# Performance work log

Measured on AMD Instinct MI355X. Metric: run time of the kernel, lower is better.

The kernel has to match this reference:

```python
import jax, jax.numpy as jnp
import numpy as np
import math

N_EMBD = 768
N_HEAD = 12
B, T = 4, 2048
HEAD_DIM = N_EMBD // N_HEAD


def new_gelu(x):
    # GPT-2 tanh approximation of GELU (NewGELUActivation)
    c = math.sqrt(2.0 / math.pi)
    return 0.5 * x * (1.0 + jnp.tanh(c * (x + 0.044715 * jnp.power(x, 3.0))))


def layer_norm(x, g, b, eps=1e-5):
    mu = jnp.mean(x, axis=-1, keepdims=True)
    var = jnp.mean(jnp.square(x - mu), axis=-1, keepdims=True)
    return (x - mu) * jax.lax.rsqrt(var + eps) * g + b


def setup_inputs() -> dict:
    key = jax.random.key(0)
    ks = jax.random.split(key, 12)
    s = 0.02
    return {
        "x": jax.random.normal(ks[0], (B, T, N_EMBD), dtype=jnp.float32),
        "ln1_g": jnp.ones((N_EMBD,), jnp.float32),
        "ln1_b": jnp.zeros((N_EMBD,), jnp.float32),
        "W_attn": jax.random.normal(ks[1], (N_EMBD, 3 * N_EMBD), jnp.float32) * s,
        "b_attn": jnp.zeros((3 * N_EMBD,), jnp.float32),
        "W_proj": jax.random.normal(ks[2], (N_EMBD, N_EMBD), jnp.float32) * s,
        "b_proj": jnp.zeros((N_EMBD,), jnp.float32),
        "ln2_g": jnp.ones((N_EMBD,), jnp.float32),
        "ln2_b": jnp.zeros((N_EMBD,), jnp.float32),
        "W_fc": jax.random.normal(ks[3], (N_EMBD, 4 * N_EMBD), jnp.float32) * s,
        "b_fc": jnp.zeros((4 * N_EMBD,), jnp.float32),
        "W_fc2": jax.random.normal(ks[4], (4 * N_EMBD, N_EMBD), jnp.float32) * s,
        "b_fc2": jnp.zeros((N_EMBD,), jnp.float32),
    }


def block_forward(x, ln1_g, ln1_b, W_attn, b_attn, W_proj, b_proj,
                  ln2_g, ln2_b, W_fc, b_fc, W_fc2, b_fc2):
    # ---- attention sublayer (pre-LN) ----
    h = layer_norm(x, ln1_g, ln1_b)
    qkv = h @ W_attn + b_attn                      # [B,T,3C]
    q, k, v = jnp.split(qkv, 3, axis=-1)
    q = q.reshape(B, T, N_HEAD, HEAD_DIM).transpose(0, 2, 1, 3)  # [B,H,T,D]
    k = k.reshape(B, T, N_HEAD, HEAD_DIM).transpose(0, 2, 1, 3)
    v = v.reshape(B, T, N_HEAD, HEAD_DIM).transpose(0, 2, 1, 3)
    scores = jnp.einsum('bhqd,bhkd->bhqk', q, k) / math.sqrt(HEAD_DIM)
    causal = jnp.tril(jnp.ones((T, T), dtype=bool))
    scores = jnp.where(causal[None, None, :, :], scores, -jnp.inf)
    attn = jax.nn.softmax(scores, axis=-1)
    y = jnp.einsum('bhqk,bhkd->bhqd', attn, v)      # [B,H,T,D]
    y = y.transpose(0, 2, 1, 3).reshape(B, T, N_EMBD)
    y = y @ W_proj + b_proj
    x = x + y
    # ---- MLP sublayer ----
    h = layer_norm(x, ln2_g, ln2_b)
    h = new_gelu(h @ W_fc + b_fc)
    h = h @ W_fc2 + b_fc2
    return x + h


def reference(x, ln1_g, ln1_b, W_attn, b_attn, W_proj, b_proj,
              ln2_g, ln2_b, W_fc, b_fc, W_fc2, b_fc2):
    return block_forward(x, ln1_g, ln1_b, W_attn, b_attn, W_proj, b_proj,
                         ln2_g, ln2_b, W_fc, b_fc, W_fc2, b_fc2)
```

## Files before the change

### kernel.cpp

```cpp
#include <hip/hip_runtime.h>
#include <hip/hip_bf16.h>

typedef __attribute__((ext_vector_type(8))) short short8;
typedef __attribute__((ext_vector_type(4))) float f32x4;
typedef __attribute__((ext_vector_type(8))) unsigned short u16x8;
typedef __attribute__((ext_vector_type(4))) unsigned short u16x4;

#define MFMA16(A, B, C) __builtin_amdgcn_mfma_f32_16x16x32_bf16(A, B, C, 0, 0, 0)

static __device__ __forceinline__ unsigned short f2bf(float f) {
    unsigned int u = __builtin_bit_cast(unsigned int, f);
    u += 0x7FFF + ((u >> 16) & 1);
    return (unsigned short)(u >> 16);
}

static __device__ __forceinline__ unsigned int cvt_pk_bf16(float a, float b) {
    unsigned int r;
    asm("v_cvt_pk_bf16_f32 %0, %1, %2" : "=v"(r) : "v"(a), "v"(b));
    return r;
}

static __device__ __forceinline__ float gelu_f(float v) {
    const float k1 = 2.3022077646f;
    const float k2 = 0.1029432207f;
    float t = __builtin_amdgcn_exp2f(-(k1 * v + k2 * v * v * v));
    return v * __builtin_amdgcn_rcpf(1.0f + t);
}

typedef const __attribute__((address_space(1))) unsigned int* gas_t;
typedef __attribute__((address_space(3))) unsigned int* las_t;
static __device__ __forceinline__ void gl_lds16(const void* g, void* l) {
    __builtin_amdgcn_global_load_lds((gas_t)g, (las_t)l, 16, 0, 0);
}

__global__ void wtrans(const float* __restrict__ W, unsigned short* __restrict__ Wt,
                       int K, int N) {
    __shared__ float tl[32][33];
    const int n0 = blockIdx.x * 32, k0 = blockIdx.y * 32;
    const int tx = threadIdx.x, ty = threadIdx.y;
#pragma unroll
    for (int i = 0; i < 4; i++)
        tl[ty + 8 * i][tx] = W[(long)(k0 + ty + 8 * i) * N + n0 + tx];
    __syncthreads();
#pragma unroll
    for (int i = 0; i < 4; i++)
        Wt[(long)(n0 + ty + 8 * i) * K + k0 + tx] = f2bf(tl[tx][ty + 8 * i]);
}

__global__ __launch_bounds__(256)
void ln_fwd(const float* __restrict__ x, const float* __restrict__ gw,
            const float* __restrict__ bw, unsigned short* __restrict__ out) {
    const int row = blockIdx.x * 4 + (threadIdx.x >> 6);
    const int ln = threadIdx.x & 63;
    const float4* xr = (const float4*)(x + (long)row * 768);
    float4 v[3];
    float s = 0.f;
#pragma unroll
    for (int j = 0; j < 3; j++) {
        v[j] = xr[ln + 64 * j];
        s += v[j].x + v[j].y + v[j].z + v[j].w;
    }
#pragma unroll
    for (int off = 32; off >= 1; off >>= 1) s += __shfl_xor(s, off);
    const float mean = s * (1.0f / 768.0f);
    float sq = 0.f;
#pragma unroll
    for (int j = 0; j < 3; j++) {
        float a = v[j].x - mean, b = v[j].y - mean, c = v[j].z - mean, d = v[j].w - mean;
        sq += a * a + b * b + c * c + d * d;
    }
#pragma unroll
    for (int off = 32; off >= 1; off >>= 1) sq += __shfl_xor(sq, off);
    const float rstd = rsqrtf(sq * (1.0f / 768.0f) + 1e-5f);
#pragma unroll
    for (int j = 0; j < 3; j++) {
        const int c = ln + 64 * j;
        float4 gg = ((const float4*)gw)[c];
        float4 bb = ((const float4*)bw)[c];
        u16x4 o;
        o[0] = f2bf((v[j].x - mean) * rstd * gg.x + bb.x);
        o[1] = f2bf((v[j].y - mean) * rstd * gg.y + bb.y);
        o[2] = f2bf((v[j].z - mean) * rstd * gg.z + bb.z);
        o[3] = f2bf((v[j].w - mean) * rstd * gg.w + bb.w);
        *(u16x4*)(out + (long)row * 768 + c * 4) = o;
    }
}

template <int MODE, int BN, int BM, int BK>
__global__ __launch_bounds__(BM * 2)
void gemm_bt(const unsigned short* __restrict__ A, const unsigned short* __restrict__ Bt,
             const float* __restrict__ bias, const float* __restrict__ resid,
             void* __restrict__ Out, unsigned short* __restrict__ vT,
             int M, int N, int K) {
    constexpr int NTH = BM * 2;
    constexpr int NW = BN / 32;
    constexpr int CHK = BK / 8;
    constexpr int BUF = (BM + BN) * BK;
    constexpr int RPP = NTH / CHK;
    constexpr int RPW = 64 / CHK;
    constexpr int PA = BM / RPP;
    constexpr int PB = BN / RPP;
    constexpr int STN = (BN == 128) ? 132 : 68;
    constexpr int SEGS = NTH / 64;
    constexpr int CPT = BN / SEGS;
    constexpr int BYTES_MAIN = 2 * BUF * 2;
    constexpr int BYTES_ST = 64 * STN * 4;
    constexpr int BYTES = BYTES_MAIN > BYTES_ST ? BYTES_MAIN : BYTES_ST;
    __shared__ char smem[BYTES];
    unsigned short* ubase = (unsigned short*)smem;
    float* st = (float*)smem;

    const int tid = threadIdx.x;
    const int wv = tid >> 6, ln = tid & 63;
    const int wm = wv >> 1, wn = wv & 1;
    const int g = ln >> 4, r = ln & 15;
    const int sr = ln / CHK, sc = ln % CHK;
    const int ssw = (BK == 32) ? (sc ^ ((sr >> 1) & 3)) : (sc ^ (sr & 7));
    const long mbase = (long)blockIdx.x * BM;
    const long nbase = (long)blockIdx.y * BN;

    f32x4 acc[4][NW];
    const f32x4 zero = {0.f, 0.f, 0.f, 0.f};
#pragma unroll
    for (int m = 0; m < 4; m++)
#pragma unroll
        for (int n = 0; n < NW; n++) acc[m][n] = zero;

    const int nt = K / BK;
#pragma unroll
    for (int p = 0; p < PA; p++)
        gl_lds16(A + (mbase + p * RPP + wv * RPW + sr) * (long)K + ssw * 8,
                 ubase + (p * RPP + wv * RPW) * BK);
#pragma unroll
    for (int p = 0; p < PB; p++)
        gl_lds16(Bt + (nbase + p * RPP + wv * RPW + sr) * (long)K + ssw * 8,
                 ubase + BM * BK + (p * RPP + wv * RPW) * BK);
    __syncthreads();

    const int cx = (r >> 1) & 3;
    const int rx = r & 7;
    for (int t = 0; t < nt; t++) {
        const unsigned short* cbuf = ubase + (t & 1) * BUF;
        if (t + 1 < nt) {
            unsigned short* nbuf = ubase + ((t + 1) & 1) * BUF;
            const long k0 = (long)(t + 1) * BK;
#pragma unroll
            for (int p = 0; p < PA; p++)
                gl_lds16(A + (mbase + p * RPP + wv * RPW + sr) * (long)K + k0 + ssw * 8,
                         nbuf + (p * RPP + wv * RPW) * BK);
#pragma unroll
            for (int p = 0; p < PB; p++)
                gl_lds16(Bt + (nbase + p * RPP + wv * RPW + sr) * (long)K + k0 + ssw * 8,
                         nbuf + BM * BK + (p * RPP + wv * RPW) * BK);
        }
        if constexpr (BK == 32) {
            short8 af[4], bfr[NW];
#pragma unroll
            for (int m = 0; m < 4; m++)
                af[m] = *(const short8*)(cbuf + (wm * 64 + m * 16 + r) * 32 + ((g ^ cx) * 8));
#pragma unroll
            for (int n = 0; n < NW; n++)
                bfr[n] = *(const short8*)(cbuf + BM * 32 + (wn * (BN / 2) + n * 16 + r) * 32 + ((g ^ cx) * 8));
#pragma unroll
            for (int m = 0; m < 4; m++)
#pragma unroll
                for (int n = 0; n < NW; n++) acc[m][n] = MFMA16(af[m], bfr[n], acc[m][n]);
        } else {
#pragma unroll
            for (int ks = 0; ks < 2; ks++) {
                short8 af[4], bfr[NW];
#pragma unroll
                for (int m = 0; m < 4; m++)
                    af[m] = *(const short8*)(cbuf + (wm * 64 + m * 16 + r) * 64 + (((g + 4 * ks) ^ rx) * 8));
#pragma unroll
                for (int n = 0; n < NW; n++)
                    bfr[n] = *(const short8*)(cbuf + BM * 64 + (wn * (BN / 2) + n * 16 + r) * 64 + (((g + 4 * ks) ^ rx) * 8));
#pragma unroll
                for (int m = 0; m < 4; m++)
#pragma unroll
                    for (int n = 0; n < NW; n++) acc[m][n] = MFMA16(af[m], bfr[n], acc[m][n]);
            }
        }
        __syncthreads();
    }

    const int tr = tid / SEGS, seg = tid % SEGS;
#pragma unroll 1
    for (int half = 0; half < BM / 64; half++) {
        __syncthreads();
        if (wm == half) {
#pragma unroll
            for (int m = 0; m < 4; m++)
#pragma unroll
                for (int n = 0; n < NW; n++)
#pragma unroll
                    for (int i = 0; i < 4; i++)
                        st[(m * 16 + g * 4 + i) * STN + wn * (BN / 2) + n * 16 + r] = acc[m][n][i];
        }
        __syncthreads();
        const long row = mbase + half * 64 + tr;
        if constexpr (MODE == 1) {
            if (nbase >= 1536) {
                constexpr int DC = NTH / 8;
                const int tc = tid & 7;
                const int d0 = tid >> 3;
                const long bb = mbase >> 11;
                const int tg0 = (int)(mbase & 2047) + half * 64 + tc * 8;
#pragma unroll
                for (int it = 0; it < 128 / DC; it++) {
                    const int dl = it * DC + d0;
                    const int h = (int)((nbase - 1536) >> 6) + (dl >> 6);
                    const int dd = dl & 63;
                    const float bc = bias[nbase + dl];
                    u16x8 o;
#pragma unroll
                    for (int j = 0; j < 8; j++)
                        o[j] = f2bf(st[(tc * 8 + j) * STN + dl] + bc);
                    *(u16x8*)(vT + ((bb * 12 + h) * 64 + dd) * 2048 + tg0) = o;
                }
            } else {
                const float qs = (nbase < 768) ? 0.18033688011112042f : 1.0f;
                const long cb = nbase + seg * CPT;
                unsigned short* op = (unsigned short*)Out + row * N + cb;
#pragma unroll
                for (int u2 = 0; u2 < CPT / 8; u2++) {
                    float4 a = *(const float4*)(st + tr * STN + seg * CPT + u2 * 8);
                    float4 b = *(const float4*)(st + tr * STN + seg * CPT + u2 * 8 + 4);
                    float4 ba = ((const float4*)bias)[(cb >> 2) + u2 * 2];
                    float4 bb2 = ((const float4*)bias)[(cb >> 2) + u2 * 2 + 1];
                    a.x = (a.x + ba.x) * qs; a.y = (a.y + ba.y) * qs;
                    a.z = (a.z + ba.z) * qs; a.w = (a.w + ba.w) * qs;
                    b.x = (b.x + bb2.x) * qs; b.y = (b.y + bb2.y) * qs;
                    b.z = (b.z + bb2.z) * qs; b.w = (b.w + bb2.w) * qs;
                    uint4 w;
                    w.x = cvt_pk_bf16(a.x, a.y);
                    w.y = cvt_pk_bf16(a.z, a.w);
                    w.z = cvt_pk_bf16(b.x, b.y);
                    w.w = cvt_pk_bf16(b.z, b.w);
                    *(uint4*)(op + u2 * 8) = w;
                }
            }
        } else if constexpr (MODE == 3) {
            const long cb = nbase + seg * CPT;
            unsigned short* op = (unsigned short*)Out + row * N + cb;
#pragma unroll
            for (int u2 = 0; u2 < CPT / 8; u2++) {
                float4 a = *(const float4*)(st + tr * STN + seg * CPT + u2 * 8);
                float4 b = *(const float4*)(st + tr * STN + seg * CPT + u2 * 8 + 4);
                float4 ba = ((const float4*)bias)[(cb >> 2) + u2 * 2];
                float4 bb2 = ((const float4*)bias)[(cb >> 2) + u2 * 2 + 1];
                a.x = gelu_f(a.x + ba.x); a.y = gelu_f(a.y + ba.y);
                a.z = gelu_f(a.z + ba.z); a.w = gelu_f(a.w + ba.w);
                b.x = gelu_f(b.x + bb2.x); b.y = gelu_f(b.y + bb2.y);
                b.z = gelu_f(b.z + bb2.z); b.w = gelu_f(b.w + bb2.w);
                uint4 w;
                w.x = cvt_pk_bf16(a.x, a.y);
                w.y = cvt_pk_bf16(a.z, a.w);
                w.z = cvt_pk_bf16(b.x, b.y);
                w.w = cvt_pk_bf16(b.z, b.w);
                *(uint4*)(op + u2 * 8) = w;
            }
        } else {
            const long cb = nbase + seg * CPT;
            float* op = (float*)Out + row * N + cb;
            const float* rp = resid + row * N + cb;
#pragma unroll
            for (int u = 0; u < CPT / 4; u++) {
                float4 a = *(const float4*)(st + tr * STN + seg * CPT + u * 4);
                float4 ba = ((const float4*)bias)[(cb >> 2) + u];
                float4 rr = ((const float4*)rp)[u];
                a.x += ba.x + rr.x; a.y += ba.y + rr.y;
                a.z += ba.z + rr.z; a.w += ba.w + rr.w;
                ((float4*)op)[u] = a;
            }
        }
    }
}

__global__ __launch_bounds__(256)
void attn_fwd(const unsigned short* __restrict__ qkv, const unsigned short* __restrict__ vT,
              unsigned short* __restrict__ y) {
    const int pair = blockIdx.x;
    const int bh = blockIdx.y;
    const int b = bh / 12, h = bh % 12;
    const int qtA = pair, qtB = 31 - pair;
    __shared__ unsigned short smem[2 * 64 * 64 + 2 * 64 * 64 + 64 * 64];
    unsigned short* Kl = smem;
    unsigned short* Vl = smem + 2 * 4096;
    unsigned short* Pl = smem + 4 * 4096;
    const int tid = threadIdx.x;
    const int wv = tid >> 6, ln = tid & 63;
    const int g = ln >> 4, r = ln & 15;
    const int lr = ln >> 3, l8 = ln & 7;
    const int sw = l8 ^ lr;
    const int rx = r & 7;
    const f32x4 zero = {0.f, 0.f, 0.f, 0.f};
    const int q = wv * 16 + r;

    const int q7 = q & 7;
    unsigned short* plw[4];
#pragma unroll
    for (int kf = 0; kf < 4; kf++)
        plw[kf] = Pl + q * 64 + ((2 * kf + (g >> 1)) ^ q7) * 8 + (g & 1) * 4;
    const unsigned short* plr0 = Pl + q * 64 + (g ^ q7) * 8;
    const unsigned short* plr1 = Pl + q * 64 + ((4 + g) ^ q7) * 8;

    const long qoffA = ((long)(b * 2048 + qtA * 64 + q)) * 2304 + h * 64;
    const long qoffB = ((long)(b * 2048 + qtB * 64 + q)) * 2304 + h * 64;
    short8 bqA0 = *(const short8*)(qkv + qoffA + g * 8);
    short8 bqA1 = *(const short8*)(qkv + qoffA + 32 + g * 8);
    short8 bqB0 = *(const short8*)(qkv + qoffB + g * 8);
    short8 bqB1 = *(const short8*)(qkv + qoffB + 32 + g * 8);

    float lA = 0.0f, lB = 0.0f;
    f32x4 oA[4], oB[4];
#pragma unroll
    for (int f = 0; f < 4; f++) { oA[f] = zero; oB[f] = zero; }

    auto process = [&](const short8& b0, const short8& b1, float& lrow,
                       f32x4* oacc, bool diag, const unsigned short* Kb,
                       const unsigned short* Vb) {
        f32x4 s[4];
#pragma unroll
        for (int kf = 0; kf < 4; kf++) {
            short8 a0 = *(const short8*)(Kb + (kf * 16 + r) * 64 + (g ^ rx) * 8);
            short8 a1 = *(const short8*)(Kb + (kf * 16 + r) * 64 + ((g + 4) ^ rx) * 8);
            s[kf] = MFMA16(a0, b0, zero);
            s[kf] = MFMA16(a1, b1, s[kf]);
        }
        if (diag) {
#pragma unroll
            for (int kf = 0; kf < 4; kf++)
#pragma unroll
                for (int i = 0; i < 4; i++)
                    if (kf * 16 + g * 4 + i > q) s[kf][i] = -1e30f;
        }
        float pv[4][4];
        float psum = 0.f;
#pragma unroll
        for (int kf = 0; kf < 4; kf++)
#pragma unroll
            for (int i = 0; i < 4; i++) {
                pv[kf][i] = __builtin_amdgcn_exp2f(s[kf][i]);
                psum += pv[kf][i];
            }
        psum += __shfl_xor(psum, 16);
        psum += __shfl_xor(psum, 32);
        lrow += psum;
#pragma unroll
        for (int kf = 0; kf < 4; kf++) {
            uint2 w;
            w.x = cvt_pk_bf16(pv[kf][0], pv[kf][1]);
            w.y = cvt_pk_bf16(pv[kf][2], pv[kf][3]);
            *(uint2*)plw[kf] = w;
        }
        short8 pb0 = *(const short8*)plr0;
        short8 pb1 = *(const short8*)plr1;
#pragma unroll
        for (int f = 0; f < 4; f++) {
            short8 va0 = *(const short8*)(Vb + (f * 16 + r) * 64 + (g ^ rx) * 8);
            short8 va1 = *(const short8*)(Vb + (f * 16 + r) * 64 + ((g + 4) ^ rx) * 8);
            oacc[f] = MFMA16(va0, pb0, oacc[f]);
            oacc[f] = MFMA16(va1, pb1, oacc[f]);
        }
    };

#pragma unroll
    for (int p = 0; p < 2; p++) {
        const int row = wv * 8 + p * 32 + lr;
        gl_lds16(qkv + ((long)(b * 2048 + row)) * 2304 + 768 + h * 64 + sw * 8,
                 (char*)Kl + (wv * 8 + p * 32) * 128);
        gl_lds16(vT + ((long)(bh * 64 + row)) * 2048 + sw * 8,
                 (char*)Vl + (wv * 8 + p * 32) * 128);
    }
    __syncthreads();

    for (int kt = 0; kt <= qtB; ++kt) {
        const unsigned short* Kb = Kl + (kt & 1) * 4096;
        const unsigned short* Vb = Vl + (kt & 1) * 4096;
        if (kt < qtB) {
            char* Kn = (char*)Kl + ((kt + 1) & 1) * 8192;
            char* Vn = (char*)Vl + ((kt + 1) & 1) * 8192;
#pragma unroll
            for (int p = 0; p < 2; p++) {
                const int row = wv * 8 + p * 32 + lr;
                gl_lds16(qkv + ((long)(b * 2048 + (kt + 1) * 64 + row)) * 2304 + 768 + h * 64 + sw * 8,
                         Kn + (wv * 8 + p * 32) * 128);
                gl_lds16(vT + ((long)(bh * 64 + row)) * 2048 + (kt + 1) * 64 + sw * 8,
                         Vn + (wv * 8 + p * 32) * 128);
            }
        }
        if (kt <= qtA) process(bqA0, bqA1, lA, oA, kt == qtA, Kb, Vb);
        process(bqB0, bqB1, lB, oB, kt == qtB, Kb, Vb);
        __syncthreads();
    }

#pragma unroll 1
    for (int e = 0; e < 2; e++) {
        const float inv = 1.0f / (e ? lB : lA);
        const f32x4* oacc = e ? oB : oA;
        const int q0 = (e ? qtB : qtA) * 64;
#pragma unroll
        for (int f = 0; f < 4; f++) {
            uint2 w;
            w.x = cvt_pk_bf16(oacc[f][0] * inv, oacc[f][1] * inv);
            w.y = cvt_pk_bf16(oacc[f][2] * inv, oacc[f][3] * inv);
            *(uint2*)plw[f] = w;
        }
        __syncthreads();
#pragma unroll
        for (int p = 0; p < 2; p++) {
            int idx = p * 256 + tid;
            int row = idx >> 3, cc = idx & 7;
            *(u16x8*)(y + ((long)(b * 2048 + q0 + row)) * 768 + h * 64 + cc * 8) =
                *(const u16x8*)(Pl + row * 64 + (cc ^ (row & 7)) * 8);
        }
        __syncthreads();
    }
}

extern "C" void kernel_launch(void* const* d_in, const int* in_sizes, int n_in,
                              void* d_out, int out_size, void* d_ws, size_t ws_size,
                              hipStream_t stream) {
    const float* x      = (const float*)d_in[0];
    const float* ln1_g  = (const float*)d_in[1];
    const float* ln1_b  = (const float*)d_in[2];
    const float* W_attn = (const float*)d_in[3];
    const float* b_attn = (const float*)d_in[4];
    const float* W_proj = (const float*)d_in[5];
    const float* b_proj = (const float*)d_in[6];
    const float* ln2_g  = (const float*)d_in[7];
    const float* ln2_b  = (const float*)d_in[8];
    const float* W_fc   = (const float*)d_in[9];
    const float* b_fc   = (const float*)d_in[10];
    const float* W_fc2  = (const float*)d_in[11];
    const float* b_fc2  = (const float*)d_in[12];

    char* ws = (char*)d_ws;
    size_t off = 0;
    auto alloc = [&](size_t bytes) -> char* {
        char* p = ws + off;
        off += (bytes + 255) & ~(size_t)255;
        return p;
    };
    unsigned short* WtA  = (unsigned short*)alloc((size_t)2304 * 768 * 2);
    unsigned short* WtP  = (unsigned short*)alloc((size_t)768 * 768 * 2);
    unsigned short* WtF  = (unsigned short*)alloc((size_t)3072 * 768 * 2);
    unsigned short* WtF2 = (unsigned short*)alloc((size_t)768 * 3072 * 2);
    unsigned short* bigA = (unsigned short*)alloc((size_t)8192 * 3072 * 2);
    float*          x1   = (float*)alloc((size_t)8192 * 768 * 4);
    unsigned short* bufD = (unsigned short*)alloc((size_t)8192 * 768 * 2);
    unsigned short* vT   = (unsigned short*)alloc((size_t)48 * 64 * 2048 * 2);

    wtrans<<<dim3(72, 24), dim3(32, 8), 0, stream>>>(W_attn, WtA, 768, 2304);
    wtrans<<<dim3(24, 24), dim3(32, 8), 0, stream>>>(W_proj, WtP, 768, 768);
    wtrans<<<dim3(96, 24), dim3(32, 8), 0, stream>>>(W_fc, WtF, 768, 3072);
    wtrans<<<dim3(24, 96), dim3(32, 8), 0, stream>>>(W_fc2, WtF2, 3072, 768);
    ln_fwd<<<2048, 256, 0, stream>>>(x, ln1_g, ln1_b, bufD);
    gemm_bt<1, 128, 256, 32><<<dim3(32, 18), 512, 0, stream>>>(bufD, WtA, b_attn, nullptr, bigA, vT, 8192, 2304, 768);
    attn_fwd<<<dim3(16, 48), 256, 0, stream>>>(bigA, vT, bufD);
    gemm_bt<2, 64, 128, 64><<<dim3(64, 12), 256, 0, stream>>>(bufD, WtP, b_proj, x, x1, nullptr, 8192, 768, 768);
    ln_fwd<<<2048, 256, 0, stream>>>(x1, ln2_g, ln2_b, bufD);
    gemm_bt<3, 128, 256, 32><<<dim3(32, 24), 512, 0, stream>>>(bufD, WtF, b_fc, nullptr, bigA, nullptr, 8192, 3072, 768);
    gemm_bt<4, 64, 128, 64><<<dim3(64, 12), 256, 0, stream>>>(bigA, WtF2, b_fc2, x1, (float*)d_out, nullptr, 8192, 768, 3072);
}
```

Baseline: 257.9 us.

## Merge weight transposes into one launch and interleave attention QK with priorities

```diff
diff --git a/kernel.cpp b/kernel.cpp
--- a/kernel.cpp
+++ b/kernel.cpp
@@ -33,11 +33,20 @@
     __builtin_amdgcn_global_load_lds((gas_t)g, (las_t)l, 16, 0, 0);
 }
 
-__global__ void wtrans(const float* __restrict__ W, unsigned short* __restrict__ Wt,
-                       int K, int N) {
+__global__ __launch_bounds__(256)
+void wtrans_all(const float* __restrict__ W0, const float* __restrict__ W1,
+                const float* __restrict__ W2, const float* __restrict__ W3,
+                unsigned short* __restrict__ T0, unsigned short* __restrict__ T1,
+                unsigned short* __restrict__ T2, unsigned short* __restrict__ T3) {
     __shared__ float tl[32][33];
-    const int n0 = blockIdx.x * 32, k0 = blockIdx.y * 32;
-    const int tx = threadIdx.x, ty = threadIdx.y;
+    const int idx = blockIdx.x;
+    const float* W; unsigned short* Wt; int K, N, nx, bx;
+    if (idx < 1728)      { W = W0; Wt = T0; K = 768;  N = 2304; bx = idx;        nx = 72; }
+    else if (idx < 2304) { W = W1; Wt = T1; K = 768;  N = 768;  bx = idx - 1728; nx = 24; }
+    else if (idx < 4608) { W = W2; Wt = T2; K = 768;  N = 3072; bx = idx - 2304; nx = 96; }
+    else                 { W = W3; Wt = T3; K = 3072; N = 768;  bx = idx - 4608; nx = 24; }
+    const int n0 = (bx % nx) * 32, k0 = (bx / nx) * 32;
+    const int tx = threadIdx.x & 31, ty = threadIdx.x >> 5;
 #pragma unroll
     for (int i = 0; i < 4; i++)
         tl[ty + 8 * i][tx] = W[(long)(k0 + ty + 8 * i) * N + n0 + tx];
@@ -317,10 +326,8 @@
 #pragma unroll
     for (int f = 0; f < 4; f++) { oA[f] = zero; oB[f] = zero; }
 
-    auto process = [&](const short8& b0, const short8& b1, float& lrow,
-                       f32x4* oacc, bool diag, const unsigned short* Kb,
-                       const unsigned short* Vb) {
-        f32x4 s[4];
+    auto qk = [&](f32x4* s, const short8& b0, const short8& b1,
+                  const unsigned short* Kb) {
 #pragma unroll
         for (int kf = 0; kf < 4; kf++) {
             short8 a0 = *(const short8*)(Kb + (kf * 16 + r) * 64 + (g ^ rx) * 8);
@@ -328,13 +335,8 @@
             s[kf] = MFMA16(a0, b0, zero);
             s[kf] = MFMA16(a1, b1, s[kf]);
         }
-        if (diag) {
-#pragma unroll
-            for (int kf = 0; kf < 4; kf++)
-#pragma unroll
-                for (int i = 0; i < 4; i++)
-                    if (kf * 16 + g * 4 + i > q) s[kf][i] = -1e30f;
-        }
+    };
+    auto smpv = [&](f32x4* s, float& lrow, f32x4* oacc, const unsigned short* Vb) {
         float pv[4][4];
         float psum = 0.f;
 #pragma unroll
@@ -356,6 +358,7 @@
         }
         short8 pb0 = *(const short8*)plr0;
         short8 pb1 = *(const short8*)plr1;
+        __builtin_amdgcn_s_setprio(1);
 #pragma unroll
         for (int f = 0; f < 4; f++) {
             short8 va0 = *(const short8*)(Vb + (f * 16 + r) * 64 + (g ^ rx) * 8);
@@ -363,6 +366,7 @@
             oacc[f] = MFMA16(va0, pb0, oacc[f]);
             oacc[f] = MFMA16(va1, pb1, oacc[f]);
         }
+        __builtin_amdgcn_s_setprio(0);
     };
 
 #pragma unroll
@@ -390,8 +394,30 @@
                          Vn + (wv * 8 + p * 32) * 128);
             }
         }
-        if (kt <= qtA) process(bqA0, bqA1, lA, oA, kt == qtA, Kb, Vb);
-        process(bqB0, bqB1, lB, oB, kt == qtB, Kb, Vb);
+        const bool doA = (kt <= qtA);
+        f32x4 sA[4], sB[4];
+        __builtin_amdgcn_s_setprio(1);
+        if (doA) qk(sA, bqA0, bqA1, Kb);
+        qk(sB, bqB0, bqB1, Kb);
+        __builtin_amdgcn_s_setprio(0);
+        if (doA) {
+            if (kt == qtA) {
+#pragma unroll
+                for (int kf = 0; kf < 4; kf++)
+#pragma unroll
+                    for (int i = 0; i < 4; i++)
+                        if (kf * 16 + g * 4 + i > q) sA[kf][i] = -1e30f;
+            }
+            smpv(sA, lA, oA, Vb);
+        }
+        if (kt == qtB) {
+#pragma unroll
+            for (int kf = 0; kf < 4; kf++)
+#pragma unroll
+                for (int i = 0; i < 4; i++)
+                    if (kf * 16 + g * 4 + i > q) sB[kf][i] = -1e30f;
+        }
+        smpv(sB, lB, oB, Vb);
         __syncthreads();
     }
 
@@ -452,10 +478,7 @@
     unsigned short* bufD = (unsigned short*)alloc((size_t)8192 * 768 * 2);
     unsigned short* vT   = (unsigned short*)alloc((size_t)48 * 64 * 2048 * 2);
 
-    wtrans<<<dim3(72, 24), dim3(32, 8), 0, stream>>>(W_attn, WtA, 768, 2304);
-    wtrans<<<dim3(24, 24), dim3(32, 8), 0, stream>>>(W_proj, WtP, 768, 768);
-    wtrans<<<dim3(96, 24), dim3(32, 8), 0, stream>>>(W_fc, WtF, 768, 3072);
-    wtrans<<<dim3(24, 96), dim3(32, 8), 0, stream>>>(W_fc2, WtF2, 3072, 768);
+    wtrans_all<<<6912, 256, 0, stream>>>(W_attn, W_proj, W_fc, W_fc2, WtA, WtP, WtF, WtF2);
     ln_fwd<<<2048, 256, 0, stream>>>(x, ln1_g, ln1_b, bufD);
     gemm_bt<1, 128, 256, 32><<<dim3(32, 18), 512, 0, stream>>>(bufD, WtA, b_attn, nullptr, bigA, vT, 8192, 2304, 768);
     attn_fwd<<<dim3(16, 48), 256, 0, stream>>>(bigA, vT, bufD);
```

Result: no change. 260.8 us (+1.1%).
